# Optimization experiments

Measured on AMD Instinct MI355X. Metric: run time of the kernel, lower is better.

Reference implementation:

```python
import jax, jax.numpy as jnp
import numpy as np

NUM_HEADS = 12
STEP_SIZE = 3

def softmax_1(a):
    # exp(a_i) / (1 + sum_j exp(a_j)), numerically stable
    m = jnp.maximum(jnp.max(a, axis=-1, keepdims=True), 0.0)
    e = jnp.exp(a - m)
    return e / (jnp.exp(-m) + jnp.sum(e, axis=-1, keepdims=True))

def setup_inputs() -> dict:
    key = jax.random.key(0)
    ks = jax.random.split(key, 7)
    B, N, C, L = 16, 4096, 768, 16
    s = C ** -0.5
    return {
        "x": jax.random.normal(ks[0], (B, N, C), dtype=jnp.float32),
        "query": jax.random.normal(ks[1], (1, L, C), dtype=jnp.float32),
        "Wq": jax.random.normal(ks[2], (C, C), dtype=jnp.float32) * s,
        "Wk": jax.random.normal(ks[3], (C, C), dtype=jnp.float32) * s,
        "Wv": jax.random.normal(ks[4], (C, C), dtype=jnp.float32) * s,
        "Wproj": jax.random.normal(ks[5], (C, C), dtype=jnp.float32) * s,
        "b_proj": jnp.zeros((C,), dtype=jnp.float32),
    }

def reference(x, query, Wq, Wk, Wv, Wproj, b_proj):
    B, N, C = x.shape
    H = NUM_HEADS
    hd = C // H
    L = query.shape[1]
    scale = hd ** -0.5
    # learned queries broadcast over batch
    queries = jnp.broadcast_to(query, (B, L, C))
    q = (queries @ Wq.T).reshape(B, L, H, hd).transpose(0, 2, 1, 3)  # [B,H,L,hd]
    k = (x @ Wk.T).reshape(B, N, H, hd).transpose(0, 2, 1, 3)        # [B,H,N,hd]
    v = k  # Hopfield update: state retrieves against stored patterns k
    for _ in range(STEP_SIZE):
        qs = q * scale
        attn = jnp.einsum('bhld,bhnd->bhln', qs, k)  # [B,H,L,N]
        attn = softmax_1(attn)
        q = jnp.einsum('bhln,bhnd->bhld', attn, v)   # [B,H,L,hd]
    out = q.transpose(0, 2, 1, 3).reshape(B, L, C)
    out = out @ Wv.T          # self.v output projection (no bias)
    out = out @ Wproj.T + b_proj  # self.proj
    return out
```

## Files before the change

kernel.cpp:

```cpp
#include <hip/hip_runtime.h>


typedef float  float4v  __attribute__((ext_vector_type(4)));
typedef short  short4v  __attribute__((ext_vector_type(4)));
typedef short  short8v  __attribute__((ext_vector_type(8)));
typedef unsigned int uint4v __attribute__((ext_vector_type(4)));
typedef short8v bf16x8;

__device__ __forceinline__ unsigned short f2bf_hi(float f){
  unsigned int u = __float_as_uint(f);
  u += 0x7fffu + ((u >> 16) & 1u);
  return (unsigned short)(u >> 16);
}
__device__ __forceinline__ float bf2f(unsigned short h){
  return __uint_as_float(((unsigned int)h) << 16);
}
__device__ __forceinline__ unsigned int packbf(float v){
  unsigned short hh = f2bf_hi(v);
  return (unsigned)hh | ((unsigned)f2bf_hi(v - bf2f(hh)) << 16);
}

__global__ __launch_bounds__(256)
void cvt_planar_kernel(const float* __restrict__ src, unsigned short* __restrict__ dh,
                       unsigned short* __restrict__ dl){
  size_t idx = (size_t)blockIdx.x*256 + threadIdx.x;
  float4v v = ((const float4v*)src)[idx];
  short4v h4, l4;
  #pragma unroll
  for(int e=0;e<4;e++){
    unsigned short hh = f2bf_hi(v[e]);
    h4[e] = (short)hh;
    l4[e] = (short)f2bf_hi(v[e] - bf2f(hh));
  }
  ((short4v*)dh)[idx] = h4;
  ((short4v*)dl)[idx] = l4;
}

__global__ __launch_bounds__(256)
void q0_kernel(const float* __restrict__ query, const float* __restrict__ wq,
               float* __restrict__ q0){
  int idx = blockIdx.x*256 + threadIdx.x;
  int l = idx / 768, c = idx - l*768;
  const float* qr = query + l*768;
  const float* wr = wq + (size_t)c*768;
  float s = 0.f;
  for(int j=0;j<768;j+=4){
    float4v a  = *(const float4v*)(qr+j);
    float4v w4 = *(const float4v*)(wr+j);
    s += a[0]*w4[0]+a[1]*w4[1]+a[2]*w4[2]+a[3]*w4[3];
  }
  q0[idx] = s;
}

__global__ __launch_bounds__(256, 4)
void gemm_k_kernel(const float* __restrict__ x, const unsigned short* __restrict__ wh,
                   const unsigned short* __restrict__ wl, unsigned int* __restrict__ khead){
  __shared__ unsigned short Ah[128*40], Al[128*40];
  const int tid  = threadIdx.x;
  const int id   = blockIdx.x;
  const int xcd  = id & 7, slot = id >> 3;
  const int bml  = slot / 6;
  const int bn   = slot - bml*6;
  const int bm   = xcd*64 + bml;
  const int wave = tid >> 6, lane = tid & 63, quad = lane >> 4, l16 = lane & 15;

  float4v acc[8][2];
  #pragma unroll
  for(int i=0;i<8;i++)
    #pragma unroll
    for(int j=0;j<2;j++) acc[i][j] = (float4v){0.f,0.f,0.f,0.f};

  const float* xA = x + (size_t)bm*128*768;
  const unsigned short* wbh = wh + (size_t)(bn*128 + wave*32 + l16)*768 + quad*8;
  const unsigned short* wbl = wl + (size_t)(bn*128 + wave*32 + l16)*768 + quad*8;

  for(int k0=0;k0<768;k0+=32){
    bf16x8 b_h[2], b_l[2];
    #pragma unroll
    for(int j=0;j<2;j++){
      b_h[j] = *(const bf16x8*)(wbh + (size_t)j*16*768 + k0);
      b_l[j] = *(const bf16x8*)(wbl + (size_t)j*16*768 + k0);
    }
    __syncthreads();
    #pragma unroll
    for(int i=0;i<2;i++){
      int fi = tid + i*256;
      int row = fi >> 2, c8 = fi & 3;
      const float* sp = xA + (size_t)row*768 + k0 + c8*8;
      float4v va = *(const float4v*)sp;
      float4v vb = *(const float4v*)(sp + 4);
      short8v hv, lv;
      #pragma unroll
      for(int e=0;e<4;e++){
        unsigned short hh = f2bf_hi(va[e]);
        hv[e] = (short)hh; lv[e] = (short)f2bf_hi(va[e] - bf2f(hh));
        unsigned short hh2 = f2bf_hi(vb[e]);
        hv[e+4] = (short)hh2; lv[e+4] = (short)f2bf_hi(vb[e] - bf2f(hh2));
      }
      *(short8v*)(Ah + row*40 + c8*8) = hv;
      *(short8v*)(Al + row*40 + c8*8) = lv;
    }
    __syncthreads();

    #pragma unroll
    for(int i=0;i<8;i++){
      const int ar = i*16 + l16;
      bf16x8 a_h = *(const bf16x8*)(Ah + ar*40 + quad*8);
      bf16x8 a_l = *(const bf16x8*)(Al + ar*40 + quad*8);
      #pragma unroll
      for(int j=0;j<2;j++){
        acc[i][j] = __builtin_amdgcn_mfma_f32_16x16x32_bf16(a_h, b_h[j], acc[i][j],0,0,0);
        acc[i][j] = __builtin_amdgcn_mfma_f32_16x16x32_bf16(a_l, b_h[j], acc[i][j],0,0,0);
        acc[i][j] = __builtin_amdgcn_mfma_f32_16x16x32_bf16(a_h, b_l[j], acc[i][j],0,0,0);
      }
    }
  }
  const int b     = bm >> 5;
  const int Cbase = bn*128 + wave*32;
  const int h     = Cbase >> 6;
  const int dbase = Cbase & 63;
  const int nn0   = (bm & 31)*128;
  unsigned int* kout = khead + ((size_t)(b*12 + h)*4096 + nn0)*64 + dbase;
  #pragma unroll
  for(int i=0;i<8;i++)
    #pragma unroll
    for(int j=0;j<2;j++)
      #pragma unroll
      for(int r=0;r<4;r++)
        kout[(size_t)(i*16 + quad*4 + r)*64 + j*16 + l16] = packbf(acc[i][j][r]);
}

__global__ __launch_bounds__(512, 2)
void attn3_kernel(const unsigned int* __restrict__ khead,
                  const float* __restrict__ q0g, float* __restrict__ qcur){
  __shared__ unsigned int knd[256*64];
  float* accf  = (float*)knd;
  float* lredf = (float*)knd + 8192;
  float* qtmp  = (float*)knd + 8320;

  const int tid  = threadIdx.x;
  const int bh   = blockIdx.x;
  const int b    = bh / 12;
  const int h    = bh - b*12;
  const int wave = tid >> 6, lane = tid & 63, quad = lane >> 4, l16 = lane & 15;

  const unsigned int* kb = khead + (size_t)(b*12 + h)*4096*64;
  const int srow = tid >> 1, scol = (tid & 1)*32;
  const int sphi = ((srow & 7) << 2) ^ ((srow & 8) << 1);
  const unsigned int* kbt = kb + (size_t)srow*64 + scol;

  const int rowA = wave*32 + ((l16 >> 2) << 3) + (l16 & 3);
  const int rowB = rowA + 4;
  const int phiA = ((l16 & 3) << 2) ^ (((l16 >> 2) & 1) << 4);
  const int phiB = phiA ^ 16;
  const int q1   = quad & 1;

  uint4v pf[8];
  #pragma unroll
  for(int g=0; g<8; ++g) pf[g] = *(const uint4v*)(kbt + g*4);

  for(int iter = 0; iter < 3; ++iter){
    const float* qrow = (iter == 0) ? (q0g + (size_t)l16*768 + h*64)
                                    : (qtmp + l16*64);
    bf16x8 qh[2], ql[2];
    #pragma unroll
    for(int s = 0; s < 2; ++s){
      float4v v0 = *(const float4v*)(qrow + s*32 + quad*8);
      float4v v1 = *(const float4v*)(qrow + s*32 + quad*8 + 4);
      #pragma unroll
      for(int e = 0; e < 8; ++e){
        float v = (e < 4 ? v0[e] : v1[e-4]) * 0.125f;
        unsigned short hh = f2bf_hi(v);
        qh[s][e] = (short)hh;
        ql[s][e] = (short)f2bf_hi(v - bf2f(hh));
      }
    }
    __syncthreads();

    float4v acc[4];
    #pragma unroll
    for(int j=0;j<4;j++) acc[j] = (float4v){0.f,0.f,0.f,0.f};
    float lsum = 0.f;

    for(int t = 0; t < 16; ++t){
      #pragma unroll
      for(int g=0; g<8; ++g)
        *(uint4v*)(knd + srow*64 + ((scol + g*4) ^ sphi)) = pf[g];
      if(!(iter == 2 && t == 15)){
        const int tn = (t + 1) & 15;
        #pragma unroll
        for(int g=0; g<8; ++g) pf[g] = *(const uint4v*)(kbt + (size_t)tn*16384 + g*4);
      }

      float4v s1 = (float4v){0.f,0.f,0.f,0.f};
      float4v s2 = (float4v){0.f,0.f,0.f,0.f};
      #pragma unroll
      for(int s = 0; s < 2; ++s){
        const int c0 = s*32 + quad*8;
        uint4v w0 = *(const uint4v*)(knd + rowA*64 + ((c0    ) ^ phiA));
        uint4v w1 = *(const uint4v*)(knd + rowA*64 + ((c0 + 4) ^ phiA));
        uint4v u0 = *(const uint4v*)(knd + rowB*64 + ((c0    ) ^ phiB));
        uint4v u1 = *(const uint4v*)(knd + rowB*64 + ((c0 + 4) ^ phiB));
        bf16x8 a1h, a1l, a2h, a2l;
        #pragma unroll
        for(int j = 0; j < 4; ++j){
          a1h[j]   = (short)(w0[j] & 0xffffu);  a1l[j]   = (short)(w0[j] >> 16);
          a1h[j+4] = (short)(w1[j] & 0xffffu);  a1l[j+4] = (short)(w1[j] >> 16);
          a2h[j]   = (short)(u0[j] & 0xffffu);  a2l[j]   = (short)(u0[j] >> 16);
          a2h[j+4] = (short)(u1[j] & 0xffffu);  a2l[j+4] = (short)(u1[j] >> 16);
        }
        s1 = __builtin_amdgcn_mfma_f32_16x16x32_bf16(a1h, qh[s], s1, 0,0,0);
        s1 = __builtin_amdgcn_mfma_f32_16x16x32_bf16(a1l, qh[s], s1, 0,0,0);
        s1 = __builtin_amdgcn_mfma_f32_16x16x32_bf16(a1h, ql[s], s1, 0,0,0);
        s2 = __builtin_amdgcn_mfma_f32_16x16x32_bf16(a2h, qh[s], s2, 0,0,0);
        s2 = __builtin_amdgcn_mfma_f32_16x16x32_bf16(a2l, qh[s], s2, 0,0,0);
        s2 = __builtin_amdgcn_mfma_f32_16x16x32_bf16(a2h, ql[s], s2, 0,0,0);
      }

      bf16x8 pa_h, pa_l;
      #pragma unroll
      for(int e = 0; e < 4; ++e){
        float v = __expf(s1[e]);
        lsum += v;
        unsigned short hh = f2bf_hi(v);
        pa_h[e] = (short)hh;
        pa_l[e] = (short)f2bf_hi(v - bf2f(hh));
        float v2 = __expf(s2[e]);
        lsum += v2;
        unsigned short hh2 = f2bf_hi(v2);
        pa_h[e+4] = (short)hh2;
        pa_l[e+4] = (short)f2bf_hi(v2 - bf2f(hh2));
      }

      const int rb0 = wave*32 + quad*8;
      #pragma unroll
      for(int j = 0; j < 4; ++j){
        bf16x8 kbh, kbl;
        #pragma unroll
        for(int e = 0; e < 8; ++e){
          const int jx = ((e >> 2) ^ q1) & 1;
          unsigned int w = knd[(rb0 + e)*64 + ((j ^ jx) << 4) + (l16 ^ ((e & 3) << 2))];
          kbh[e] = (short)(w & 0xffffu);
          kbl[e] = (short)(w >> 16);
        }
        acc[j] = __builtin_amdgcn_mfma_f32_16x16x32_bf16(pa_h, kbh, acc[j], 0,0,0);
        acc[j] = __builtin_amdgcn_mfma_f32_16x16x32_bf16(pa_l, kbh, acc[j], 0,0,0);
        acc[j] = __builtin_amdgcn_mfma_f32_16x16x32_bf16(pa_h, kbl, acc[j], 0,0,0);
      }
    }

    __syncthreads();
    lsum += __shfl_xor(lsum, 16);
    lsum += __shfl_xor(lsum, 32);
    if(quad == 0) lredf[wave*16 + l16] = lsum;
    #pragma unroll
    for(int j = 0; j < 4; ++j)
      #pragma unroll
      for(int r = 0; r < 4; ++r)
        accf[wave*1024 + (quad*4 + r)*64 + j*16 + l16] = acc[j][r];
    __syncthreads();
    #pragma unroll
    for(int k = 0; k < 2; ++k){
      const int i = tid + k*512;
      const int l = i >> 6, d = i & 63;
      float s = 0.f, lt = 1.f;
      #pragma unroll
      for(int w = 0; w < 8; ++w){ s += accf[w*1024 + i]; }
      #pragma unroll
      for(int w = 0; w < 8; ++w){ lt += lredf[w*16 + l]; }
      const float qv = s / lt;
      if(iter < 2) qtmp[i] = qv;
      else qcur[(size_t)(b*16 + l)*768 + h*64 + d] = qv;
    }
    __syncthreads();
  }
}

__global__ __launch_bounds__(256)
void proj_kernel(const float* __restrict__ inp, const float* __restrict__ w,
                 const float* __restrict__ bias, float* __restrict__ out){
  __shared__ float rows[4*768];
  const int r0 = blockIdx.x*4;
  const int c  = blockIdx.y*256 + threadIdx.x;
  for(int j = threadIdx.x; j < 4*768; j += 256) rows[j] = inp[(size_t)r0*768 + j];
  __syncthreads();
  const float* wr = w + (size_t)c*768;
  float a0=0.f, a1=0.f, a2=0.f, a3=0.f;
  for(int j=0;j<768;j+=4){
    float4v w4 = *(const float4v*)(wr+j);
    float4v r0v = *(const float4v*)(rows+j);
    float4v r1v = *(const float4v*)(rows+768+j);
    float4v r2v = *(const float4v*)(rows+1536+j);
    float4v r3v = *(const float4v*)(rows+2304+j);
    #pragma unroll
    for(int e=0;e<4;e++){
      a0 += r0v[e]*w4[e]; a1 += r1v[e]*w4[e];
      a2 += r2v[e]*w4[e]; a3 += r3v[e]*w4[e];
    }
  }
  const float bb = bias ? bias[c] : 0.f;
  out[(size_t)(r0+0)*768 + c] = a0 + bb;
  out[(size_t)(r0+1)*768 + c] = a1 + bb;
  out[(size_t)(r0+2)*768 + c] = a2 + bb;
  out[(size_t)(r0+3)*768 + c] = a3 + bb;
}

extern "C" void kernel_launch(void* const* d_in, const int* in_sizes, int n_in,
                              void* d_out, int out_size, void* d_ws, size_t ws_size,
                              hipStream_t stream){
  const float* x     = (const float*)d_in[0];
  const float* query = (const float*)d_in[1];
  const float* Wq    = (const float*)d_in[2];
  const float* Wk    = (const float*)d_in[3];
  const float* Wv    = (const float*)d_in[4];
  const float* Wproj = (const float*)d_in[5];
  const float* bproj = (const float*)d_in[6];
  float* out = (float*)d_out;

  char* ws = (char*)d_ws;
  unsigned int*   khead = (unsigned int*)(ws);
  float*          qcur  = (float*)(ws + 201326592);
  float*          q0    = (float*)(ws + 202113024);
  char*           R     = ws + 202162176;
  unsigned short* wkh   = (unsigned short*)(R);
  unsigned short* wkl   = (unsigned short*)(R + 1179648);
  float*          out1  = (float*)(R);

  cvt_planar_kernel<<<576, 256, 0, stream>>>(Wk, wkh, wkl);
  q0_kernel<<<48, 256, 0, stream>>>(query, Wq, q0);
  gemm_k_kernel<<<3072, 256, 0, stream>>>(x, wkh, wkl, khead);

  attn3_kernel<<<192, 512, 0, stream>>>(khead, q0, qcur);

  proj_kernel<<<dim3(64, 3), 256, 0, stream>>>(qcur, Wv, nullptr, out1);
  proj_kernel<<<dim3(64, 3), 256, 0, stream>>>(out1, Wproj, bproj, out);
}
```

Before: 713.7 us.

## Prefetch x tiles into registers, swizzle LDS layout, cheapen bf16 split

The K-projection GEMM now loads the next x tile into registers while the MFMAs for the current tile run. It replaces the padded LDS rows with an XOR-swizzled 16-byte chunk layout and lowers the occupancy hint from 4 to 3 blocks per CU. Everywhere, the bf16 hi/lo split now truncates the high half instead of rounding it, and rounds only the low residual, which saves integer ops. The extra prefetch registers and the lower occupancy may cost latency hiding, and the truncated high part slightly changes the split arithmetic.

```diff
diff --git a/kernel.cpp b/kernel.cpp
--- a/kernel.cpp
+++ b/kernel.cpp
@@ -7,17 +7,16 @@
 typedef unsigned int uint4v __attribute__((ext_vector_type(4)));
 typedef short8v bf16x8;
 
-__device__ __forceinline__ unsigned short f2bf_hi(float f){
-  unsigned int u = __float_as_uint(f);
-  u += 0x7fffu + ((u >> 16) & 1u);
-  return (unsigned short)(u >> 16);
-}
-__device__ __forceinline__ float bf2f(unsigned short h){
-  return __uint_as_float(((unsigned int)h) << 16);
+__device__ __forceinline__ void splitbf(float v, unsigned int& hi, unsigned int& lo){
+  unsigned int u = __float_as_uint(v);
+  hi = u >> 16;
+  float r = v - __uint_as_float(u & 0xffff0000u);
+  lo = (__float_as_uint(r) + 0x8000u) >> 16;
 }
 __device__ __forceinline__ unsigned int packbf(float v){
-  unsigned short hh = f2bf_hi(v);
-  return (unsigned)hh | ((unsigned)f2bf_hi(v - bf2f(hh)) << 16);
+  unsigned int u = __float_as_uint(v);
+  float r = v - __uint_as_float(u & 0xffff0000u);
+  return (u >> 16) | ((__float_as_uint(r) + 0x8000u) & 0xffff0000u);
 }
 
 __global__ __launch_bounds__(256)
@@ -28,9 +27,10 @@
   short4v h4, l4;
   #pragma unroll
   for(int e=0;e<4;e++){
-    unsigned short hh = f2bf_hi(v[e]);
+    unsigned int hh, ll;
+    splitbf(v[e], hh, ll);
     h4[e] = (short)hh;
-    l4[e] = (short)f2bf_hi(v[e] - bf2f(hh));
+    l4[e] = (short)ll;
   }
   ((short4v*)dh)[idx] = h4;
   ((short4v*)dl)[idx] = l4;
@@ -52,10 +52,10 @@
   q0[idx] = s;
 }
 
-__global__ __launch_bounds__(256, 4)
+__global__ __launch_bounds__(256, 3)
 void gemm_k_kernel(const float* __restrict__ x, const unsigned short* __restrict__ wh,
                    const unsigned short* __restrict__ wl, unsigned int* __restrict__ khead){
-  __shared__ unsigned short Ah[128*40], Al[128*40];
+  __shared__ unsigned short Ah[512*8], Al[512*8];
   const int tid  = threadIdx.x;
   const int id   = blockIdx.x;
   const int xcd  = id & 7, slot = id >> 3;
@@ -74,6 +74,18 @@
   const unsigned short* wbh = wh + (size_t)(bn*128 + wave*32 + l16)*768 + quad*8;
   const unsigned short* wbl = wl + (size_t)(bn*128 + wave*32 + l16)*768 + quad*8;
 
+  const int row0 = tid >> 2, c8 = tid & 3;
+  const int C0 = row0*4 + (c8 ^ ((row0 >> 2) & 3));
+  const int C1 = C0 + 256;
+  const float* g0 = xA + (size_t)row0*768 + c8*8;
+  const float* g1 = g0 + (size_t)64*768;
+  const int crd = l16*4 + (quad ^ ((l16 >> 2) & 3));
+
+  float4v p00 = *(const float4v*)(g0);
+  float4v p01 = *(const float4v*)(g0 + 4);
+  float4v p10 = *(const float4v*)(g1);
+  float4v p11 = *(const float4v*)(g1 + 4);
+
   for(int k0=0;k0<768;k0+=32){
     bf16x8 b_h[2], b_l[2];
     #pragma unroll
@@ -82,31 +94,41 @@
       b_l[j] = *(const bf16x8*)(wbl + (size_t)j*16*768 + k0);
     }
     __syncthreads();
-    #pragma unroll
-    for(int i=0;i<2;i++){
-      int fi = tid + i*256;
-      int row = fi >> 2, c8 = fi & 3;
-      const float* sp = xA + (size_t)row*768 + k0 + c8*8;
-      float4v va = *(const float4v*)sp;
-      float4v vb = *(const float4v*)(sp + 4);
+
+    {
       short8v hv, lv;
       #pragma unroll
       for(int e=0;e<4;e++){
-        unsigned short hh = f2bf_hi(va[e]);
-        hv[e] = (short)hh; lv[e] = (short)f2bf_hi(va[e] - bf2f(hh));
-        unsigned short hh2 = f2bf_hi(vb[e]);
-        hv[e+4] = (short)hh2; lv[e+4] = (short)f2bf_hi(vb[e] - bf2f(hh2));
-      }
-      *(short8v*)(Ah + row*40 + c8*8) = hv;
-      *(short8v*)(Al + row*40 + c8*8) = lv;
-    }
-    __syncthreads();
+        unsigned int hh, ll;
+        splitbf(p00[e], hh, ll); hv[e]   = (short)hh; lv[e]   = (short)ll;
+        splitbf(p01[e], hh, ll); hv[e+4] = (short)hh; lv[e+4] = (short)ll;
+      }
+      *(short8v*)(Ah + C0*8) = hv;
+      *(short8v*)(Al + C0*8) = lv;
+      #pragma unroll
+      for(int e=0;e<4;e++){
+        unsigned int hh, ll;
+        splitbf(p10[e], hh, ll); hv[e]   = (short)hh; lv[e]   = (short)ll;
+        splitbf(p11[e], hh, ll); hv[e+4] = (short)hh; lv[e+4] = (short)ll;
+      }
+      *(short8v*)(Ah + C1*8) = hv;
+      *(short8v*)(Al + C1*8) = lv;
+    }
+    __syncthreads();
+
+    if(k0 + 32 < 768){
+      p00 = *(const float4v*)(g0 + k0 + 32);
+      p01 = *(const float4v*)(g0 + k0 + 36);
+      p10 = *(const float4v*)(g1 + k0 + 32);
+      p11 = *(const float4v*)(g1 + k0 + 36);
+    }
 
     #pragma unroll
     for(int i=0;i<8;i++){
-      const int ar = i*16 + l16;
-      bf16x8 a_h = *(const bf16x8*)(Ah + ar*40 + quad*8);
-      bf16x8 a_l = *(const bf16x8*)(Al + ar*40 + quad*8);
+      const unsigned short* ap = Ah + (size_t)(i*64 + crd)*8;
+      const unsigned short* lp = Al + (size_t)(i*64 + crd)*8;
+      bf16x8 a_h = *(const bf16x8*)ap;
+      bf16x8 a_l = *(const bf16x8*)lp;
       #pragma unroll
       for(int j=0;j<2;j++){
         acc[i][j] = __builtin_amdgcn_mfma_f32_16x16x32_bf16(a_h, b_h[j], acc[i][j],0,0,0);
@@ -170,9 +192,10 @@
       #pragma unroll
       for(int e = 0; e < 8; ++e){
         float v = (e < 4 ? v0[e] : v1[e-4]) * 0.125f;
-        unsigned short hh = f2bf_hi(v);
+        unsigned int hh, ll;
+        splitbf(v, hh, ll);
         qh[s][e] = (short)hh;
-        ql[s][e] = (short)f2bf_hi(v - bf2f(hh));
+        ql[s][e] = (short)ll;
       }
     }
     __syncthreads();
@@ -222,14 +245,15 @@
       for(int e = 0; e < 4; ++e){
         float v = __expf(s1[e]);
         lsum += v;
-        unsigned short hh = f2bf_hi(v);
+        unsigned int hh, ll;
+        splitbf(v, hh, ll);
         pa_h[e] = (short)hh;
-        pa_l[e] = (short)f2bf_hi(v - bf2f(hh));
+        pa_l[e] = (short)ll;
         float v2 = __expf(s2[e]);
         lsum += v2;
-        unsigned short hh2 = f2bf_hi(v2);
-        pa_h[e+4] = (short)hh2;
-        pa_l[e+4] = (short)f2bf_hi(v2 - bf2f(hh2));
+        splitbf(v2, hh, ll);
+        pa_h[e+4] = (short)hh;
+        pa_l[e+4] = (short)ll;
       }
 
       const int rb0 = wave*32 + quad*8;
```

Measured after the change: 682.6 us. 1.05x faster.
